# Performance work log

Measured on AMD Instinct MI355X. Metric: run time of the kernel, lower is better.

Reference implementation:

```python
import jax, jax.numpy as jnp
import numpy as np

N_SRC, N_DST, N_EDGES = 50000, 50000, 500000
IN_DIM, OUT_DIM, EDGE_DIM = 128, 128, 11
BN_EPS = 1e-5


def setup_inputs() -> dict:
    key = jax.random.key(0)
    ks = jax.random.split(key, 16)
    s = 0.05
    return {
        "src_feat": jax.random.normal(ks[0], (N_SRC, IN_DIM), jnp.float32),
        "dst_feat": jax.random.normal(ks[1], (N_DST, IN_DIM), jnp.float32),
        "edge_feats": jax.random.normal(ks[2], (N_EDGES, EDGE_DIM), jnp.float32),
        "src_idx": jax.random.randint(ks[3], (N_EDGES,), 0, N_SRC, jnp.int32),
        "dst_idx": jax.random.randint(ks[4], (N_EDGES,), 0, N_DST, jnp.int32),
        "W_src": jax.random.normal(ks[5], (IN_DIM, OUT_DIM), jnp.float32) * s,
        "b_src": jnp.zeros((OUT_DIM,), jnp.float32),
        "W_dst": jax.random.normal(ks[6], (IN_DIM, OUT_DIM), jnp.float32) * s,
        "b_dst": jnp.zeros((OUT_DIM,), jnp.float32),
        "W_edge": jax.random.normal(ks[7], (EDGE_DIM, OUT_DIM), jnp.float32) * s,
        "b_edge": jnp.zeros((OUT_DIM,), jnp.float32),
        "attn_w": jax.random.normal(ks[8], (3 * OUT_DIM,), jnp.float32) * s,
        "attn_b": jnp.zeros((), jnp.float32),
        "gamma": jnp.ones((OUT_DIM,), jnp.float32),
        "beta": jnp.zeros((OUT_DIM,), jnp.float32),
        "alpha": jnp.asarray(0.25, jnp.float32),
    }


def reference(src_feat, dst_feat, edge_feats, src_idx, dst_idx,
              W_src, b_src, W_dst, b_dst, W_edge, b_edge,
              attn_w, attn_b, gamma, beta, alpha):
    D = W_src.shape[1]
    # project at node/edge level (math identical to projecting gathered feats)
    hs = src_feat @ W_src + b_src            # [Ns, D]  (linear_src)
    hd = dst_feat @ W_dst + b_dst            # [Nd, D]  (linear_dst)
    ep = edge_feats @ W_edge + b_edge        # [E, D]   (linear_edge)
    # attn_l on concat([src, dst, edge]) == sum of three dot products + bias
    aw_s, aw_d, aw_e = attn_w[:D], attn_w[D:2 * D], attn_w[2 * D:]
    a = (hs @ aw_s)[src_idx] + (hd @ aw_d)[dst_idx] + ep @ aw_e + attn_b  # [E]
    # edge softmax over incoming edges of each dst node
    n_dst = dst_feat.shape[0]
    seg_max = jax.ops.segment_max(a, dst_idx, num_segments=n_dst)
    a_exp = jnp.exp(a - seg_max[dst_idx])
    denom = jax.ops.segment_sum(a_exp, dst_idx, num_segments=n_dst)
    attn = a_exp / denom[dst_idx]            # [E]
    # weighted message = attn * linear_src(src_h); scatter-sum to dst
    msg = attn[:, None] * hs[src_idx]        # [E, D]
    h_new = jax.ops.segment_sum(msg, dst_idx, num_segments=n_dst)  # [Nd, D]
    # BatchNorm1d (training-mode batch statistics)
    mean = jnp.mean(h_new, axis=0)
    var = jnp.var(h_new, axis=0)
    h_bn = (h_new - mean) / jnp.sqrt(var + BN_EPS) * gamma + beta
    # PReLU (single shared alpha); dropout is identity in eval
    return jnp.where(h_bn >= 0, h_bn, alpha * h_bn)
```

## Files before the change

### kernel.cpp

```cpp
#include <hip/hip_runtime.h>
#include <cstddef>

#define NSRC 50000
#define NDST 50000
#define NEDGE 500000
#define DIM 128
#define EDIM 11
#define BN_EPS 1e-5f
#define SCAN_NBLK ((NDST + 255) / 256)

#define HS_BLOCKS ((NSRC + 63) / 64)
#define DS_BLOCKS ((NDST + 31) / 32)
#define ED_BLOCKS ((NEDGE + 1023) / 1024)

typedef short bf16x8 __attribute__((ext_vector_type(8)));
typedef float f32x4 __attribute__((ext_vector_type(4)));

#define OFF_HS       0
#define OFF_SSCORE   (OFF_HS + (size_t)NSRC*DIM/2)
#define OFF_DSCORE   (OFF_SSCORE + NSRC)
#define OFF_EE       (OFF_DSCORE + NDST)
#define OFF_DEG16    (OFF_EE + NEDGE)
#define OFF_COLSUM   (OFF_DEG16 + (size_t)NDST*16)
#define OFF_COLSQ    (OFF_COLSUM + 128)
#define OFF_OFFS     (OFF_COLSQ + 128)
#define OFF_CUR16    (OFF_OFFS + NDST + 2)
#define OFF_PAIRS    (OFF_CUR16 + (size_t)NDST*16)
#define OFF_WDVEC    (OFF_PAIRS + 2*(size_t)NEDGE)
#define OFF_WEVEC    (OFF_WDVEC + 128)
#define OFF_SCAL     (OFF_WEVEC + 16)
#define OFF_PART     (OFF_SCAL + 4)
#define OFF_WT       (((OFF_PART + 256 + 3) / 4) * 4)

__device__ __forceinline__ unsigned short f2bf(float x) {
    unsigned int u = __float_as_uint(x);
    u += 0x7FFFu + ((u >> 16) & 1u);
    return (unsigned short)(u >> 16);
}
__device__ __forceinline__ float bf2f(unsigned int u16) {
    return __uint_as_float(u16 << 16);
}

__global__ void k_prep(const float* __restrict__ W_dst, const float* __restrict__ b_dst,
                       const float* __restrict__ W_edge, const float* __restrict__ b_edge,
                       const float* __restrict__ attn_w, const float* __restrict__ attn_b,
                       float* __restrict__ wd_vec, float* __restrict__ we_vec,
                       float* __restrict__ scal) {
    int t = threadIdx.x;
    float acc = 0.f;
    for (int d = 0; d < DIM; ++d) acc += W_dst[t * DIM + d] * attn_w[DIM + d];
    wd_vec[t] = acc;
    if (t < EDIM) {
        float e = 0.f;
        for (int d = 0; d < DIM; ++d) e += W_edge[t * DIM + d] * attn_w[2 * DIM + d];
        we_vec[t] = e;
    }
    __shared__ float red[128];
    red[t] = b_dst[t] * attn_w[DIM + t];
    __syncthreads();
    for (int s = 64; s > 0; s >>= 1) { if (t < s) red[t] += red[t + s]; __syncthreads(); }
    if (t == 0) scal[0] = red[0];
    __syncthreads();
    red[t] = b_edge[t] * attn_w[2 * DIM + t];
    __syncthreads();
    for (int s = 64; s > 0; s >>= 1) { if (t < s) red[t] += red[t + s]; __syncthreads(); }
    if (t == 0) scal[1] = red[0] + attn_b[0];
}

__global__ __launch_bounds__(256) void k_wt(const float* __restrict__ W,
                                            unsigned short* __restrict__ wt) {
    __shared__ float tile[32][33];
    int bi = blockIdx.x & 3;
    int bj = blockIdx.x >> 2;
    int t = threadIdx.x;
    int cl = t & 31;
    #pragma unroll
    for (int i = 0; i < 4; ++i) {
        int kl = (t >> 5) * 4 + i;
        tile[kl][cl] = W[(size_t)(bi * 32 + kl) * DIM + bj * 32 + cl];
    }
    __syncthreads();
    int ko = t & 31;
    #pragma unroll
    for (int i = 0; i < 4; ++i) {
        int co = (t >> 5) * 4 + i;
        wt[(size_t)(bj * 32 + co) * DIM + bi * 32 + ko] = f2bf(tile[ko][co]);
    }
}

__global__ __launch_bounds__(256, 2) void k_fused(const float* __restrict__ A,
                                               const unsigned short* __restrict__ wt,
                                               const float* __restrict__ bias,
                                               const float* __restrict__ attn_w,
                                               const float* __restrict__ B,
                                               const float* __restrict__ ef,
                                               const int* __restrict__ dst_idx,
                                               const float* __restrict__ wd_vec,
                                               const float* __restrict__ we_vec,
                                               const float* __restrict__ scal,
                                               unsigned short* __restrict__ hsb,
                                               float* __restrict__ s_score,
                                               float* __restrict__ d_score,
                                               float* __restrict__ ee,
                                               int* __restrict__ deg16) {
    const int bid = blockIdx.x;
    const int t = threadIdx.x;

    if (bid < HS_BLOCKS) {
        const int wv = t >> 6;
        const int lane = t & 63;
        const int lrow = lane & 15;
        const int kg = lane >> 4;
        const int grow = bid * 64 + wv * 16 + lrow;
        const bool rowok = grow < NSRC;
        const float* arow = A + (size_t)grow * DIM;

        bf16x8 af[4];
        #pragma unroll
        for (int s = 0; s < 4; ++s) {
            float4 p0 = make_float4(0.f, 0.f, 0.f, 0.f), p1 = p0;
            if (rowok) {
                p0 = *reinterpret_cast<const float4*>(arow + 32 * s + kg * 8);
                p1 = *reinterpret_cast<const float4*>(arow + 32 * s + kg * 8 + 4);
            }
            bf16x8 a;
            a[0] = (short)f2bf(p0.x); a[1] = (short)f2bf(p0.y);
            a[2] = (short)f2bf(p0.z); a[3] = (short)f2bf(p0.w);
            a[4] = (short)f2bf(p1.x); a[5] = (short)f2bf(p1.y);
            a[6] = (short)f2bf(p1.z); a[7] = (short)f2bf(p1.w);
            af[s] = a;
        }

        f32x4 acc[8];
        #pragma unroll
        for (int c = 0; c < 8; ++c) acc[c] = (f32x4){0.f, 0.f, 0.f, 0.f};

        #pragma unroll
        for (int c = 0; c < 8; ++c) {
            #pragma unroll
            for (int s = 0; s < 4; ++s) {
                const bf16x8 b = *reinterpret_cast<const bf16x8*>(
                    wt + ((size_t)(16 * c + lrow) * DIM + 32 * s + kg * 8));
                acc[c] = __builtin_amdgcn_mfma_f32_16x16x32_bf16(af[s], b, acc[c], 0, 0, 0);
            }
        }

        float p[4] = {0.f, 0.f, 0.f, 0.f};
        #pragma unroll
        for (int c = 0; c < 8; ++c) {
            float bb = bias[16 * c + lrow];
            float aw = attn_w[16 * c + lrow];
            #pragma unroll
            for (int i = 0; i < 4; ++i) {
                float v = acc[c][i] + bb;
                acc[c][i] = v;
                p[i] += v * aw;
            }
        }
        #pragma unroll
        for (int i = 0; i < 4; ++i) {
            p[i] += __shfl_xor(p[i], 1);
            p[i] += __shfl_xor(p[i], 2);
            p[i] += __shfl_xor(p[i], 4);
            p[i] += __shfl_xor(p[i], 8);
        }
        const int orow0 = bid * 64 + wv * 16 + kg * 4;
        #pragma unroll
        for (int i = 0; i < 4; ++i) {
            int orow = orow0 + i;
            if (orow < NSRC) {
                #pragma unroll
                for (int c = 0; c < 8; ++c)
                    hsb[(size_t)orow * DIM + 16 * c + lrow] = f2bf(acc[c][i]);
                if (lrow == 0) s_score[orow] = p[i];
            }
        }
    } else if (bid < HS_BLOCKS + DS_BLOCKS) {
        int row = (bid - HS_BLOCKS) * 32 + (t >> 3);
        int c0 = (t & 7) * 16;
        if (row >= NDST) return;
        const float4* x = reinterpret_cast<const float4*>(B + (size_t)row * DIM + c0);
        const float4* w = reinterpret_cast<const float4*>(wd_vec + c0);
        float p = 0.f;
        #pragma unroll
        for (int i = 0; i < 4; ++i) {
            float4 a = x[i], b = w[i];
            p += a.x * b.x + a.y * b.y + a.z * b.z + a.w * b.w;
        }
        p += __shfl_xor(p, 1);
        p += __shfl_xor(p, 2);
        p += __shfl_xor(p, 4);
        if ((t & 7) == 0) d_score[row] = p + scal[0];
    } else {
        float wvv[EDIM];
        #pragma unroll
        for (int k = 0; k < EDIM; ++k) wvv[k] = we_vec[k];
        const float s1 = scal[1];
        int ebase = (bid - HS_BLOCKS - DS_BLOCKS) * 1024 + t;
        #pragma unroll
        for (int i = 0; i < 4; ++i) {
            int e = ebase + i * 256;
            if (e < NEDGE) {
                const float* er = ef + (size_t)e * EDIM;
                float a = s1;
                #pragma unroll
                for (int k = 0; k < EDIM; ++k) a += er[k] * wvv[k];
                ee[e] = a;
                atomicAdd(&deg16[(size_t)dst_idx[e] * 16], 1);
            }
        }
    }
}

__global__ __launch_bounds__(256) void k_scanA(const int* __restrict__ deg16,
                                               int* __restrict__ off,
                                               int* __restrict__ partials) {
    __shared__ int tmp[256];
    int t = threadIdx.x;
    int i = blockIdx.x * 256 + t;
    int v = (i < NDST) ? deg16[(size_t)i * 16] : 0;
    tmp[t] = v;
    __syncthreads();
    #pragma unroll
    for (int d = 1; d < 256; d <<= 1) {
        int u = (t >= d) ? tmp[t - d] : 0;
        __syncthreads();
        tmp[t] += u;
        __syncthreads();
    }
    if (i < NDST) off[i] = tmp[t] - v;
    if (t == 255) partials[blockIdx.x] = tmp[255];
}

__global__ __launch_bounds__(256) void k_scanB(int* __restrict__ partials) {
    __shared__ int tmp[256];
    int t = threadIdx.x;
    int v = (t < SCAN_NBLK) ? partials[t] : 0;
    tmp[t] = v;
    __syncthreads();
    #pragma unroll
    for (int d = 1; d < 256; d <<= 1) {
        int u = (t >= d) ? tmp[t - d] : 0;
        __syncthreads();
        tmp[t] += u;
        __syncthreads();
    }
    if (t < SCAN_NBLK) partials[t] = tmp[t] - v;
}

__global__ __launch_bounds__(256) void k_scanC(int* __restrict__ off,
                                               int* __restrict__ cur16,
                                               const int* __restrict__ partials) {
    int t = threadIdx.x;
    int i = blockIdx.x * 256 + t;
    if (i < NDST) {
        int f = off[i] + partials[blockIdx.x];
        off[i] = f;
        cur16[(size_t)i * 16] = f;
    }
    if (i == 0) off[NDST] = NEDGE;
}

__global__ __launch_bounds__(256) void k_scat(const int* __restrict__ src_idx,
                                              const int* __restrict__ dst_idx,
                                              const float* __restrict__ ee,
                                              const float* __restrict__ s_score,
                                              const float* __restrict__ d_score,
                                              int* __restrict__ cur16,
                                              int2* __restrict__ pairs) {
    int base = blockIdx.x * 1024 + threadIdx.x;
    #pragma unroll
    for (int i = 0; i < 4; ++i) {
        int e = base + i * 256;
        if (e < NEDGE) {
            int s = src_idx[e], d = dst_idx[e];
            float w = expf(ee[e] + s_score[s] + d_score[d]);
            int pos = atomicAdd(&cur16[(size_t)d * 16], 1);
            pairs[pos] = make_int2(s, __float_as_int(w));
        }
    }
}

__global__ __launch_bounds__(256) void k_gather(const unsigned short* __restrict__ hsb,
                                                const int* __restrict__ off,
                                                const int2* __restrict__ pairs,
                                                float* __restrict__ h_new) {
    int wid = (blockIdx.x * blockDim.x + threadIdx.x) >> 6;
    int lane = threadIdx.x & 63;
    if (wid >= NDST) return;
    int b = off[wid], e2 = off[wid + 1];
    int deg = e2 - b;
    float ax = 0.f, ay = 0.f, wsum = 0.f;

    for (int base = 0; base < deg; base += 64) {
        int cnt = min(deg - base, 64);
        int myS = 0;
        float myW = 0.f;
        if (lane < cnt) {
            int2 p = pairs[b + base + lane];
            myS = p.x;
            myW = __int_as_float(p.y);
        }
        wsum += myW;

        int j = 0;
        for (; j + 4 <= cnt; j += 4) {
            int s0 = __shfl(myS, j + 0), s1 = __shfl(myS, j + 1);
            int s2 = __shfl(myS, j + 2), s3 = __shfl(myS, j + 3);
            float w0 = __shfl(myW, j + 0), w1 = __shfl(myW, j + 1);
            float w2 = __shfl(myW, j + 2), w3 = __shfl(myW, j + 3);
            unsigned int v0 = *reinterpret_cast<const unsigned int*>(hsb + (size_t)s0 * DIM + 2 * lane);
            unsigned int v1 = *reinterpret_cast<const unsigned int*>(hsb + (size_t)s1 * DIM + 2 * lane);
            unsigned int v2 = *reinterpret_cast<const unsigned int*>(hsb + (size_t)s2 * DIM + 2 * lane);
            unsigned int v3 = *reinterpret_cast<const unsigned int*>(hsb + (size_t)s3 * DIM + 2 * lane);
            ax += w0 * bf2f(v0 & 0xFFFFu) + w1 * bf2f(v1 & 0xFFFFu)
                + w2 * bf2f(v2 & 0xFFFFu) + w3 * bf2f(v3 & 0xFFFFu);
            ay += w0 * bf2f(v0 >> 16) + w1 * bf2f(v1 >> 16)
                + w2 * bf2f(v2 >> 16) + w3 * bf2f(v3 >> 16);
        }
        for (; j < cnt; ++j) {
            int s0 = __shfl(myS, j);
            float w0 = __shfl(myW, j);
            unsigned int v0 = *reinterpret_cast<const unsigned int*>(hsb + (size_t)s0 * DIM + 2 * lane);
            ax += w0 * bf2f(v0 & 0xFFFFu);
            ay += w0 * bf2f(v0 >> 16);
        }
    }

    #pragma unroll
    for (int m = 1; m < 64; m <<= 1) wsum += __shfl_xor(wsum, m);

    float inv = (deg > 0) ? 1.f / wsum : 0.f;
    reinterpret_cast<float2*>(h_new + (size_t)wid * DIM)[lane] = make_float2(ax * inv, ay * inv);
}

__global__ __launch_bounds__(256) void k_bnstats(const float* __restrict__ h,
                                                 float* __restrict__ colsum,
                                                 float* __restrict__ colsq) {
    int col = threadIdx.x & 127;
    int rp = threadIdx.x >> 7;
    float s = 0.f, q = 0.f;
    for (int r = blockIdx.x * 2 + rp; r < NDST; r += gridDim.x * 2) {
        float x = h[(size_t)r * DIM + col];
        s += x;
        q += x * x;
    }
    __shared__ float ls[2][128], lq[2][128];
    ls[rp][col] = s;
    lq[rp][col] = q;
    __syncthreads();
    if (rp == 0) {
        atomicAdd(&colsum[col], ls[0][col] + ls[1][col]);
        atomicAdd(&colsq[col], lq[0][col] + lq[1][col]);
    }
}

__global__ __launch_bounds__(256) void k_bnfinal(float* __restrict__ h,
                                                 const float* __restrict__ colsum,
                                                 const float* __restrict__ colsq,
                                                 const float* __restrict__ gamma,
                                                 const float* __restrict__ beta,
                                                 const float* __restrict__ alpha_p) {
    const size_t total4 = (size_t)NDST * DIM / 4;
    const float alpha = alpha_p[0];
    const float invN = 1.f / (float)NDST;
    const int c0 = (threadIdx.x & 31) * 4;
    float sc[4], sh[4];
    #pragma unroll
    for (int k = 0; k < 4; ++k) {
        float mean = colsum[c0 + k] * invN;
        float var = colsq[c0 + k] * invN - mean * mean;
        float s = gamma[c0 + k] * rsqrtf(var + BN_EPS);
        sc[k] = s;
        sh[k] = beta[c0 + k] - mean * s;
    }
    size_t stride = (size_t)gridDim.x * blockDim.x;
    for (size_t i = blockIdx.x * blockDim.x + threadIdx.x; i < total4; i += stride) {
        float4 x = reinterpret_cast<float4*>(h)[i];
        float y0 = x.x * sc[0] + sh[0];
        float y1 = x.y * sc[1] + sh[1];
        float y2 = x.z * sc[2] + sh[2];
        float y3 = x.w * sc[3] + sh[3];
        float4 o;
        o.x = y0 >= 0.f ? y0 : alpha * y0;
        o.y = y1 >= 0.f ? y1 : alpha * y1;
        o.z = y2 >= 0.f ? y2 : alpha * y2;
        o.w = y3 >= 0.f ? y3 : alpha * y3;
        reinterpret_cast<float4*>(h)[i] = o;
    }
}

extern "C" void kernel_launch(void* const* d_in, const int* in_sizes, int n_in,
                              void* d_out, int out_size, void* d_ws, size_t ws_size,
                              hipStream_t stream) {
    const float* src_feat   = (const float*)d_in[0];
    const float* dst_feat   = (const float*)d_in[1];
    const float* edge_feats = (const float*)d_in[2];
    const int*   src_idx    = (const int*)d_in[3];
    const int*   dst_idx    = (const int*)d_in[4];
    const float* W_src      = (const float*)d_in[5];
    const float* b_src      = (const float*)d_in[6];
    const float* W_dst      = (const float*)d_in[7];
    const float* b_dst      = (const float*)d_in[8];
    const float* W_edge     = (const float*)d_in[9];
    const float* b_edge     = (const float*)d_in[10];
    const float* attn_w     = (const float*)d_in[11];
    const float* attn_b     = (const float*)d_in[12];
    const float* gamma      = (const float*)d_in[13];
    const float* beta       = (const float*)d_in[14];
    const float* alpha      = (const float*)d_in[15];

    float* ws      = (float*)d_ws;
    unsigned short* hsb = (unsigned short*)(ws + OFF_HS);
    float* s_score = ws + OFF_SSCORE;
    float* d_score = ws + OFF_DSCORE;
    float* ee      = ws + OFF_EE;
    int*   deg16   = (int*)(ws + OFF_DEG16);
    float* colsum  = ws + OFF_COLSUM;
    float* colsq   = ws + OFF_COLSQ;
    int*   off     = (int*)(ws + OFF_OFFS);
    int*   cur16   = (int*)(ws + OFF_CUR16);
    int2*  pairs   = (int2*)(ws + OFF_PAIRS);
    float* wd_vec  = ws + OFF_WDVEC;
    float* we_vec  = ws + OFF_WEVEC;
    float* scal    = ws + OFF_SCAL;
    int*   part    = (int*)(ws + OFF_PART);
    unsigned short* wt = (unsigned short*)(ws + OFF_WT);

    float* h_new = (float*)d_out;

    hipMemsetAsync(deg16, 0, ((size_t)NDST * 16 + 256) * sizeof(int), stream);

    k_prep<<<1, 128, 0, stream>>>(W_dst, b_dst, W_edge, b_edge, attn_w, attn_b,
                                  wd_vec, we_vec, scal);
    k_wt<<<16, 256, 0, stream>>>(W_src, wt);
    k_fused<<<HS_BLOCKS + DS_BLOCKS + ED_BLOCKS, 256, 0, stream>>>(
        src_feat, wt, b_src, attn_w, dst_feat, edge_feats, dst_idx,
        wd_vec, we_vec, scal, hsb, s_score, d_score, ee, deg16);
    k_scanA<<<SCAN_NBLK, 256, 0, stream>>>(deg16, off, part);
    k_scanB<<<1, 256, 0, stream>>>(part);
    k_scanC<<<SCAN_NBLK, 256, 0, stream>>>(off, cur16, part);
    k_scat<<<ED_BLOCKS, 256, 0, stream>>>(src_idx, dst_idx, ee, s_score, d_score,
                                          cur16, pairs);
    k_gather<<<(NDST * 64 + 255) / 256, 256, 0, stream>>>(hsb, off, pairs, h_new);
    k_bnstats<<<512, 256, 0, stream>>>(h_new, colsum, colsq);
    k_bnfinal<<<1024, 256, 0, stream>>>(h_new, colsum, colsq, gamma, beta, alpha);
}
```

Before: 157.6 us.

## Record atomic rank during degree count to drop scatter atomics; pack bf16 stores

The degree-counting atomic in the fused kernel now saves its return value as a per-edge rank, so the scatter kernel computes each slot as off[d]+rank[e] with no second atomic pass over a cursor array. The cursor array and its initialisation in the scan are removed. The hs bf16 output is written as paired 32-bit stores using a lane shuffle instead of 16-bit stores, and the edge branch of the fused kernel uses half as many edges per block. The cost is an extra 2 MB rank array that is written once and read once.

```diff
diff --git a/kernel.cpp b/kernel.cpp
--- a/kernel.cpp
+++ b/kernel.cpp
@@ -11,7 +11,8 @@
 
 #define HS_BLOCKS ((NSRC + 63) / 64)
 #define DS_BLOCKS ((NDST + 31) / 32)
-#define ED_BLOCKS ((NEDGE + 1023) / 1024)
+#define ED_BLOCKS ((NEDGE + 511) / 512)
+#define SC_BLOCKS ((NEDGE + 1023) / 1024)
 
 typedef short bf16x8 __attribute__((ext_vector_type(8)));
 typedef float f32x4 __attribute__((ext_vector_type(4)));
@@ -24,8 +25,8 @@
 #define OFF_COLSUM   (OFF_DEG16 + (size_t)NDST*16)
 #define OFF_COLSQ    (OFF_COLSUM + 128)
 #define OFF_OFFS     (OFF_COLSQ + 128)
-#define OFF_CUR16    (OFF_OFFS + NDST + 2)
-#define OFF_PAIRS    (OFF_CUR16 + (size_t)NDST*16)
+#define OFF_RANK     (OFF_OFFS + NDST + 2)
+#define OFF_PAIRS    (OFF_RANK + NEDGE)
 #define OFF_WDVEC    (OFF_PAIRS + 2*(size_t)NEDGE)
 #define OFF_WEVEC    (OFF_WDVEC + 128)
 #define OFF_SCAL     (OFF_WEVEC + 16)
@@ -102,7 +103,8 @@
                                                float* __restrict__ s_score,
                                                float* __restrict__ d_score,
                                                float* __restrict__ ee,
-                                               int* __restrict__ deg16) {
+                                               int* __restrict__ deg16,
+                                               int* __restrict__ rank) {
     const int bid = blockIdx.x;
     const int t = threadIdx.x;
 
@@ -166,14 +168,22 @@
         }
         const int orow0 = bid * 64 + wv * 16 + kg * 4;
         #pragma unroll
+        for (int c = 0; c < 8; ++c) {
+            #pragma unroll
+            for (int i = 0; i < 4; ++i) {
+                unsigned int mybf = f2bf(acc[c][i]);
+                unsigned int nb = (unsigned int)__shfl_xor((int)mybf, 1);
+                int orow = orow0 + i;
+                if ((lrow & 1) == 0 && orow < NSRC) {
+                    *reinterpret_cast<unsigned int*>(hsb + (size_t)orow * DIM + 16 * c + lrow)
+                        = (mybf & 0xFFFFu) | (nb << 16);
+                }
+            }
+        }
+        #pragma unroll
         for (int i = 0; i < 4; ++i) {
             int orow = orow0 + i;
-            if (orow < NSRC) {
-                #pragma unroll
-                for (int c = 0; c < 8; ++c)
-                    hsb[(size_t)orow * DIM + 16 * c + lrow] = f2bf(acc[c][i]);
-                if (lrow == 0) s_score[orow] = p[i];
-            }
+            if (lrow == 0 && orow < NSRC) s_score[orow] = p[i];
         }
     } else if (bid < HS_BLOCKS + DS_BLOCKS) {
         int row = (bid - HS_BLOCKS) * 32 + (t >> 3);
@@ -196,9 +206,9 @@
         #pragma unroll
         for (int k = 0; k < EDIM; ++k) wvv[k] = we_vec[k];
         const float s1 = scal[1];
-        int ebase = (bid - HS_BLOCKS - DS_BLOCKS) * 1024 + t;
-        #pragma unroll
-        for (int i = 0; i < 4; ++i) {
+        int ebase = (bid - HS_BLOCKS - DS_BLOCKS) * 512 + t;
+        #pragma unroll
+        for (int i = 0; i < 2; ++i) {
             int e = ebase + i * 256;
             if (e < NEDGE) {
                 const float* er = ef + (size_t)e * EDIM;
@@ -206,7 +216,8 @@
                 #pragma unroll
                 for (int k = 0; k < EDIM; ++k) a += er[k] * wvv[k];
                 ee[e] = a;
-                atomicAdd(&deg16[(size_t)dst_idx[e] * 16], 1);
+                int d = dst_idx[e];
+                rank[e] = atomicAdd(&deg16[(size_t)d * 16], 1);
             }
         }
     }
@@ -249,15 +260,10 @@
 }
 
 __global__ __launch_bounds__(256) void k_scanC(int* __restrict__ off,
-                                               int* __restrict__ cur16,
                                                const int* __restrict__ partials) {
     int t = threadIdx.x;
     int i = blockIdx.x * 256 + t;
-    if (i < NDST) {
-        int f = off[i] + partials[blockIdx.x];
-        off[i] = f;
-        cur16[(size_t)i * 16] = f;
-    }
+    if (i < NDST) off[i] += partials[blockIdx.x];
     if (i == 0) off[NDST] = NEDGE;
 }
 
@@ -266,7 +272,8 @@
                                               const float* __restrict__ ee,
                                               const float* __restrict__ s_score,
                                               const float* __restrict__ d_score,
-                                              int* __restrict__ cur16,
+                                              const int* __restrict__ off,
+                                              const int* __restrict__ rank,
                                               int2* __restrict__ pairs) {
     int base = blockIdx.x * 1024 + threadIdx.x;
     #pragma unroll
@@ -275,7 +282,7 @@
         if (e < NEDGE) {
             int s = src_idx[e], d = dst_idx[e];
             float w = expf(ee[e] + s_score[s] + d_score[d]);
-            int pos = atomicAdd(&cur16[(size_t)d * 16], 1);
+            int pos = off[d] + rank[e];
             pairs[pos] = make_int2(s, __float_as_int(w));
         }
     }
@@ -419,7 +426,7 @@
     float* colsum  = ws + OFF_COLSUM;
     float* colsq   = ws + OFF_COLSQ;
     int*   off     = (int*)(ws + OFF_OFFS);
-    int*   cur16   = (int*)(ws + OFF_CUR16);
+    int*   rank    = (int*)(ws + OFF_RANK);
     int2*  pairs   = (int2*)(ws + OFF_PAIRS);
     float* wd_vec  = ws + OFF_WDVEC;
     float* we_vec  = ws + OFF_WEVEC;
@@ -436,12 +443,12 @@
     k_wt<<<16, 256, 0, stream>>>(W_src, wt);
     k_fused<<<HS_BLOCKS + DS_BLOCKS + ED_BLOCKS, 256, 0, stream>>>(
         src_feat, wt, b_src, attn_w, dst_feat, edge_feats, dst_idx,
-        wd_vec, we_vec, scal, hsb, s_score, d_score, ee, deg16);
+        wd_vec, we_vec, scal, hsb, s_score, d_score, ee, deg16, rank);
     k_scanA<<<SCAN_NBLK, 256, 0, stream>>>(deg16, off, part);
     k_scanB<<<1, 256, 0, stream>>>(part);
-    k_scanC<<<SCAN_NBLK, 256, 0, stream>>>(off, cur16, part);
-    k_scat<<<ED_BLOCKS, 256, 0, stream>>>(src_idx, dst_idx, ee, s_score, d_score,
-                                          cur16, pairs);
+    k_scanC<<<SCAN_NBLK, 256, 0, stream>>>(off, part);
+    k_scat<<<SC_BLOCKS, 256, 0, stream>>>(src_idx, dst_idx, ee, s_score, d_score,
+                                          off, rank, pairs);
     k_gather<<<(NDST * 64 + 255) / 256, 256, 0, stream>>>(hsb, off, pairs, h_new);
     k_bnstats<<<512, 256, 0, stream>>>(h_new, colsum, colsq);
     k_bnfinal<<<1024, 256, 0, stream>>>(h_new, colsum, colsq, gamma, beta, alpha);
```

New measurement: 142.8 us. 1.1x faster.
